# Optimization experiments

Measured on AMD Instinct MI355X. Metric: run time of the kernel, lower is better.

Reference implementation:

```python
import jax, jax.numpy as jnp
import numpy as np

M, K, N, R = 8192, 4096, 4096, 64  # tokens, in_features, out_features, pod_rank


def _unpack_int4(packed):
    """Unpack bytes (stored as int32 in [0,256)) into signed int4 values in [-8,7].
    Low nibble is element 2k, high nibble is element 2k+1."""
    b = packed.astype(jnp.int32)
    low = ((b & 0xF) ^ 8) - 8
    high = (((b >> 4) & 0xF) ^ 8) - 8
    out = jnp.stack([low, high], axis=-1)
    return out.reshape(packed.shape[:-1] + (packed.shape[-1] * 2,))


def setup_inputs() -> dict:
    key = jax.random.key(0)
    ks = jax.random.split(key, 7)
    x_quant = jax.random.randint(ks[0], (M, K // 2), 0, 256, dtype=jnp.int32)
    x_scale = jax.random.uniform(ks[1], (M,), dtype=jnp.float32) * 0.01 + 1e-4
    weight = jax.random.randint(ks[2], (N, K // 2), 0, 256, dtype=jnp.int32)
    weight_scales = jax.random.uniform(ks[3], (N, 1), dtype=jnp.float32) * 0.01 + 1e-4
    bias = jax.random.normal(ks[4], (N,), dtype=jnp.float32) * 0.02
    x_r = jax.random.normal(ks[5], (M, R), dtype=jnp.float32)
    w_outlier = jax.random.normal(ks[6], (N, R), dtype=jnp.float32) * 0.02
    return {"x_quant": x_quant, "x_scale": x_scale, "weight": weight,
            "weight_scales": weight_scales, "bias": bias, "x_r": x_r,
            "w_outlier": w_outlier}


def reference(x_quant, x_scale, weight, weight_scales, bias, x_r, w_outlier):
    xi = _unpack_int4(x_quant)          # [M, K] int32 in [-8,7]
    wi = _unpack_int4(weight)           # [N, K] int32 in [-8,7]
    y_int = jnp.matmul(xi, wi.T)        # [M, N] int32 accumulator
    # dequant: per-token activation scale * per-channel weight scale, plus bias
    y = (y_int.astype(jnp.float32) * x_scale[:, None] * weight_scales.reshape(1, -1)
         + bias[None, :])
    # fused low-rank outlier correction: addmm_(x_r, w_outlier.T)
    y = y + jnp.matmul(x_r, w_outlier.T)
    return y
```

## Files before the change

kernel.cpp:

```cpp
#include <hip/hip_runtime.h>
#include <hip/hip_fp16.h>

typedef int      v4i __attribute__((ext_vector_type(4)));
typedef int      v2i __attribute__((ext_vector_type(2)));
typedef float    v4f __attribute__((ext_vector_type(4)));
typedef _Float16 v8h __attribute__((ext_vector_type(8)));
typedef _Float16 v4h __attribute__((ext_vector_type(4)));

#define MDIM 8192
#define NDIM 4096
#define KDIM 4096
#define RDIM 64
#define KW   (KDIM / 2)
#define NT   (KDIM / 128)

typedef const __attribute__((address_space(1))) char* gas_ptr;
typedef __attribute__((address_space(3))) char*       las_ptr;

__device__ __forceinline__ void unpack_w(v4i w, int& lo8, int& hi8) {
    unsigned p01 = __builtin_amdgcn_perm((unsigned)w.y, (unsigned)w.x, 0x0C0C0400u);
    unsigned p23 = __builtin_amdgcn_perm((unsigned)w.w, (unsigned)w.z, 0x0C0C0400u);
    unsigned b4  = __builtin_amdgcn_perm(p23, p01, 0x05040100u);
    unsigned lo = b4 & 0x0F0F0F0Fu;
    unsigned hi = (b4 >> 4) & 0x0F0F0F0Fu;
    lo8 = (int)(((lo ^ 0x08080808u) + 0x78787878u) ^ 0x80808080u);
    hi8 = (int)(((hi ^ 0x08080808u) + 0x78787878u) ^ 0x80808080u);
}

__global__ __launch_bounds__(256)
void repack_int4(const int* __restrict__ xq, const int* __restrict__ wq,
                 char* __restrict__ x8, char* __restrict__ w8)
{
    const size_t XCH = (size_t)MDIM * KW / 4;
    const size_t TCH = XCH + (size_t)NDIM * KW / 4;
    size_t stride = (size_t)gridDim.x * blockDim.x;
    for (size_t i = (size_t)blockIdx.x * blockDim.x + threadIdx.x; i < TCH; i += stride) {
        const int* src;
        char* dst;
        if (i < XCH) { src = xq + i * 4; dst = x8 + i * 8; }
        else { size_t j = i - XCH; src = wq + j * 4; dst = w8 + j * 8; }
        v4i w = *(const v4i*)src;
        int lo8, hi8;
        unpack_w(w, lo8, hi8);
        *(v2i*)dst = (v2i){lo8, hi8};
    }
}

__device__ __forceinline__ void stage2(const char* g, char* l, int kt, int ks) {
    const char* s = g + kt * 128 + ks * 64;
    __builtin_amdgcn_global_load_lds((gas_ptr)(const void*)s,
                                     (las_ptr)(void*)l, 16, 0, 0);
    __builtin_amdgcn_global_load_lds((gas_ptr)(const void*)(s + (size_t)128 * KDIM),
                                     (las_ptr)(void*)(l + 8192), 16, 0, 0);
}

#define VM4 asm volatile("s_waitcnt vmcnt(4)" ::: "memory")
#define NOPW

#define PHASE(PAR, MH, KS, STAGE_STMT, WAIT_STMT) do {                          \
    const char* Ab = &Asub[PAR][KS][0];                                         \
    const char* Bb = &Bsub[PAR][KS][0];                                         \
    v4i a_[4], b_[4];                                                           \
    _Pragma("unroll")                                                           \
    for (int ii = 0; ii < 4; ++ii)                                              \
        a_[ii] = *(const v4i*)(Ab + aoff + ((MH) * 4 + ii) * 1024);             \
    _Pragma("unroll")                                                           \
    for (int jj = 0; jj < 4; ++jj)                                              \
        b_[jj] = *(const v4i*)(Bb + boff + jj * 1024);                          \
    STAGE_STMT;                                                                 \
    __builtin_amdgcn_s_barrier();                                               \
    __builtin_amdgcn_s_setprio(1);                                              \
    _Pragma("unroll")                                                           \
    for (int ii = 0; ii < 4; ++ii)                                              \
        _Pragma("unroll")                                                       \
        for (int jj = 0; jj < 4; ++jj)                                          \
            acc[(MH) * 4 + ii][jj] = __builtin_amdgcn_mfma_i32_16x16x64_i8(     \
                a_[ii], b_[jj], acc[(MH) * 4 + ii][jj], 0, 0, 0);               \
    __builtin_amdgcn_s_setprio(0);                                              \
    WAIT_STMT;                                                                  \
    asm volatile("s_barrier" ::: "memory");                                     \
} while (0)

__global__ __launch_bounds__(512, 2)
void w4a4_gemm8(const char* __restrict__ x8, const char* __restrict__ w8,
                const float* __restrict__ xsc, const float* __restrict__ wsc,
                const float* __restrict__ bias, const float* __restrict__ xr,
                const float* __restrict__ wo, float* __restrict__ out)
{
    __shared__ __align__(16) char Asub[2][2][16384];
    __shared__ __align__(16) char Bsub[2][2][16384];
    __shared__ float xs_s[256];
    __shared__ float ws_s[256];
    __shared__ float bs_s[256];

    const int tid  = threadIdx.x;
    const int lane = tid & 63;
    const int wid  = tid >> 6;
    const int wm   = wid >> 2;
    const int wn   = wid & 3;

    const int s  = (blockIdx.x & 7) * 64 + (blockIdx.x >> 3);
    const int by = s >> 4;
    const int bx = s & 15;

    if (tid < 256) {
        xs_s[tid] = xsc[by * 256 + tid];
    } else {
        int n = tid - 256;
        ws_s[n] = wsc[bx * 256 + n];
        bs_s[n] = bias[bx * 256 + n];
    }

    const int srow = wid * 16 + (lane >> 2);
    const int scol = ((lane & 3) * 16) ^ (((lane >> 3) & 3) << 4);
    const char* gA = x8 + (size_t)(by * 256 + srow) * KDIM + scol;
    const char* gB = w8 + (size_t)(bx * 256 + srow) * KDIM + scol;
    const int ldsW = wid * 1024;

    const int lr   = lane & 15;
    const int cef  = ((lane >> 4) << 4) ^ (((lr >> 1) & 3) << 4);
    const int aoff = (wm * 128 + lr) * 64 + cef;
    const int boff = (wn * 64  + lr) * 64 + cef;

    v4i acc[8][4];
#pragma unroll
    for (int i = 0; i < 8; ++i)
#pragma unroll
        for (int j = 0; j < 4; ++j) acc[i][j] = (v4i){0, 0, 0, 0};

    stage2(gA, &Asub[0][0][ldsW], 0, 0);
    stage2(gB, &Bsub[0][0][ldsW], 0, 0);
    stage2(gA, &Asub[0][1][ldsW], 0, 1);
    stage2(gB, &Bsub[0][1][ldsW], 0, 1);
    stage2(gA, &Asub[1][0][ldsW], 1, 0);
    stage2(gB, &Bsub[1][0][ldsW], 1, 0);
    asm volatile("s_waitcnt vmcnt(4)" ::: "memory");
    asm volatile("s_barrier" ::: "memory");

    for (int it = 0; it < NT / 2; ++it) {
        const int kt1 = 2 * it + 1;
        const int kt2 = (2 * it + 2 < NT) ? 2 * it + 2 : NT - 1;
        const int kt3 = (2 * it + 3 < NT) ? 2 * it + 3 : NT - 1;
        PHASE(0, 0, 0, stage2(gA, &Asub[1][1][ldsW], kt1, 1), NOPW);
        PHASE(0, 1, 0, stage2(gB, &Bsub[1][1][ldsW], kt1, 1), NOPW);
        PHASE(0, 0, 1, stage2(gA, &Asub[0][0][ldsW], kt2, 0), NOPW);
        PHASE(0, 1, 1, stage2(gB, &Bsub[0][0][ldsW], kt2, 0), VM4);
        PHASE(1, 0, 0, stage2(gA, &Asub[0][1][ldsW], kt2, 1), NOPW);
        PHASE(1, 1, 0, stage2(gB, &Bsub[0][1][ldsW], kt2, 1), NOPW);
        PHASE(1, 0, 1, stage2(gA, &Asub[1][0][ldsW], kt3, 0), NOPW);
        PHASE(1, 1, 1, stage2(gB, &Bsub[1][0][ldsW], kt3, 0), VM4);
    }

    asm volatile("s_waitcnt vmcnt(0)" ::: "memory");
    asm volatile("s_barrier" ::: "memory");

    _Float16* Xh = (_Float16*)&Asub[0][0][0];
    _Float16* Wh = (_Float16*)&Bsub[0][0][0];
    {
        const int rr = tid >> 3;
        const int c8 = (tid & 7) * 8;
#pragma unroll
        for (int p = 0; p < 4; ++p) {
            const int row = p * 64 + rr;
            v4f x0 = *(const v4f*)(xr + (size_t)(by * 256 + row) * RDIM + c8);
            v4f x1 = *(const v4f*)(xr + (size_t)(by * 256 + row) * RDIM + c8 + 4);
            v8h hx = {(_Float16)x0[0], (_Float16)x0[1], (_Float16)x0[2], (_Float16)x0[3],
                      (_Float16)x1[0], (_Float16)x1[1], (_Float16)x1[2], (_Float16)x1[3]};
            *(v8h*)((char*)Xh + (size_t)row * 144 + c8 * 2) = hx;
            v4f w0 = *(const v4f*)(wo + (size_t)(bx * 256 + row) * RDIM + c8);
            v4f w1 = *(const v4f*)(wo + (size_t)(bx * 256 + row) * RDIM + c8 + 4);
            v8h hw = {(_Float16)w0[0], (_Float16)w0[1], (_Float16)w0[2], (_Float16)w0[3],
                      (_Float16)w1[0], (_Float16)w1[1], (_Float16)w1[2], (_Float16)w1[3]};
            *(v8h*)((char*)Wh + (size_t)row * 144 + c8 * 2) = hw;
        }
    }

#pragma unroll
    for (int i = 0; i < 8; ++i) {
        const int r0 = wm * 128 + i * 16 + ((lane >> 4) << 2);
        const v4f xs4 = *(const v4f*)&xs_s[r0];
#pragma unroll
        for (int j = 0; j < 4; ++j) {
            const int col = wn * 64 + j * 16 + lr;
            const float sw = ws_s[col];
            const float bz = bs_s[col];
            v4f f;
#pragma unroll
            for (int r = 0; r < 4; ++r)
                f[r] = (float)acc[i][j][r] * xs4[r] * sw + bz;
            acc[i][j] = __builtin_bit_cast(v4i, f);
        }
    }
    __syncthreads();

#pragma unroll
    for (int ks = 0; ks < 2; ++ks) {
        v8h ah[8], bh[4];
#pragma unroll
        for (int i = 0; i < 8; ++i)
            ah[i] = *(const v8h*)((const char*)Xh +
                     (size_t)(wm * 128 + i * 16 + lr) * 144 + ks * 64 + ((lane >> 4) << 4));
#pragma unroll
        for (int j = 0; j < 4; ++j)
            bh[j] = *(const v8h*)((const char*)Wh +
                     (size_t)(wn * 64 + j * 16 + lr) * 144 + ks * 64 + ((lane >> 4) << 4));
#pragma unroll
        for (int i = 0; i < 8; ++i)
#pragma unroll
            for (int j = 0; j < 4; ++j) {
                v4f c = __builtin_bit_cast(v4f, acc[i][j]);
                c = __builtin_amdgcn_mfma_f32_16x16x32_f16(ah[i], bh[j], c, 0, 0, 0);
                acc[i][j] = __builtin_bit_cast(v4i, c);
            }
    }

    const size_t obase = (size_t)(by * 256 + wm * 128 + ((lane >> 4) << 2)) * NDIM
                       + bx * 256 + wn * 64 + lr;
#pragma unroll
    for (int i = 0; i < 8; ++i)
#pragma unroll
        for (int j = 0; j < 4; ++j) {
            v4f f = __builtin_bit_cast(v4f, acc[i][j]);
#pragma unroll
            for (int r = 0; r < 4; ++r)
                out[obase + (size_t)(i * 16 + r) * NDIM + j * 16] = f[r];
        }
}

__global__ __launch_bounds__(256, 2)
void w4a4_fused(const int* __restrict__ xq, const float* __restrict__ xsc,
                const int* __restrict__ wq, const float* __restrict__ wsc,
                const float* __restrict__ bias, const float* __restrict__ xr,
                const float* __restrict__ wo, float* __restrict__ out)
{
    __shared__ __align__(16) char As[128 * 144];
    __shared__ __align__(16) char Bs[128 * 144];
    __shared__ float xs_s[128];
    __shared__ float ws_s[128];
    __shared__ float bs_s[128];

    const int tid  = threadIdx.x;
    const int lane = tid & 63;
    const int wid  = tid >> 6;
    const int wm   = wid >> 1;
    const int wn   = wid & 1;
    const int bx   = blockIdx.x % (NDIM / 128);
    const int by   = blockIdx.x / (NDIM / 128);

    const int srow   = tid >> 4;
    const int schunk = tid & 15;

    if (tid < 128) {
        xs_s[tid] = xsc[by * 128 + tid];
    } else {
        int n = tid - 128;
        ws_s[n] = wsc[bx * 128 + n];
        bs_s[n] = bias[bx * 128 + n];
    }

    const int* gA = xq + (size_t)(by * 128 + srow) * KW + schunk * 4;
    const int* gB = wq + (size_t)(bx * 128 + srow) * KW + schunk * 4;
    char* lA = As + srow * 144 + schunk * 8;
    char* lB = Bs + srow * 144 + schunk * 8;

    v4i acc[4][4];
#pragma unroll
    for (int i = 0; i < 4; ++i)
#pragma unroll
        for (int j = 0; j < 4; ++j) acc[i][j] = (v4i){0, 0, 0, 0};

    const int lr = lane & 15;
    const int lkb = (lane >> 4) * 16;

    for (int kt = 0; kt < KDIM / 128; ++kt) {
#pragma unroll
        for (int p = 0; p < 8; ++p) {
            v4i w = *(const v4i*)(gA + (size_t)p * 16 * KW + kt * 64);
            int lo8, hi8;
            unpack_w(w, lo8, hi8);
            *(v2i*)(lA + p * 16 * 144) = (v2i){lo8, hi8};
        }
#pragma unroll
        for (int p = 0; p < 8; ++p) {
            v4i w = *(const v4i*)(gB + (size_t)p * 16 * KW + kt * 64);
            int lo8, hi8;
            unpack_w(w, lo8, hi8);
            *(v2i*)(lB + p * 16 * 144) = (v2i){lo8, hi8};
        }
        __syncthreads();
#pragma unroll
        for (int ks = 0; ks < 2; ++ks) {
            v4i av[4], bv[4];
#pragma unroll
            for (int i = 0; i < 4; ++i)
                av[i] = *(const v4i*)(As + (wm * 64 + i * 16 + lr) * 144 + ks * 64 + lkb);
#pragma unroll
            for (int j = 0; j < 4; ++j)
                bv[j] = *(const v4i*)(Bs + (wn * 64 + j * 16 + lr) * 144 + ks * 64 + lkb);
#pragma unroll
            for (int i = 0; i < 4; ++i)
#pragma unroll
                for (int j = 0; j < 4; ++j)
                    acc[i][j] = __builtin_amdgcn_mfma_i32_16x16x64_i8(av[i], bv[j], acc[i][j], 0, 0, 0);
        }
        __syncthreads();
    }

    _Float16* Xh = (_Float16*)As;
    _Float16* Wh = (_Float16*)Bs;
#pragma unroll
    for (int p = 0; p < 8; ++p) {
        int row = p * 16 + srow;
        float4 vx = *(const float4*)(xr + (size_t)(by * 128 + row) * RDIM + schunk * 4);
        *(v4h*)(Xh + row * 72 + schunk * 4) =
            (v4h){(_Float16)vx.x, (_Float16)vx.y, (_Float16)vx.z, (_Float16)vx.w};
        float4 vw = *(const float4*)(wo + (size_t)(bx * 128 + row) * RDIM + schunk * 4);
        *(v4h*)(Wh + row * 72 + schunk * 4) =
            (v4h){(_Float16)vw.x, (_Float16)vw.y, (_Float16)vw.z, (_Float16)vw.w};
    }
    __syncthreads();

    v4f facc[4][4];
#pragma unroll
    for (int i = 0; i < 4; ++i)
#pragma unroll
        for (int j = 0; j < 4; ++j) facc[i][j] = (v4f){0.f, 0.f, 0.f, 0.f};

    const int lkh = (lane >> 4) * 8;
#pragma unroll
    for (int ks = 0; ks < 2; ++ks) {
        v8h ah[4], bh[4];
#pragma unroll
        for (int i = 0; i < 4; ++i)
            ah[i] = *(const v8h*)(Xh + (wm * 64 + i * 16 + lr) * 72 + ks * 32 + lkh);
#pragma unroll
        for (int j = 0; j < 4; ++j)
            bh[j] = *(const v8h*)(Wh + (wn * 64 + j * 16 + lr) * 72 + ks * 32 + lkh);
#pragma unroll
        for (int i = 0; i < 4; ++i)
#pragma unroll
            for (int j = 0; j < 4; ++j)
                facc[i][j] = __builtin_amdgcn_mfma_f32_16x16x32_f16(ah[i], bh[j], facc[i][j], 0, 0, 0);
    }

#pragma unroll
    for (int i = 0; i < 4; ++i) {
        int row0 = wm * 64 + i * 16 + (lane >> 4) * 4;
#pragma unroll
        for (int j = 0; j < 4; ++j) {
            int col = wn * 64 + j * 16 + lr;
            float sw = ws_s[col];
            float bz = bs_s[col];
#pragma unroll
            for (int r = 0; r < 4; ++r) {
                int row = row0 + r;
                float v = (float)acc[i][j][r] * xs_s[row] * sw + bz + facc[i][j][r];
                out[(size_t)(by * 128 + row) * NDIM + (bx * 128 + col)] = v;
            }
        }
    }
}

extern "C" void kernel_launch(void* const* d_in, const int* in_sizes, int n_in,
                              void* d_out, int out_size, void* d_ws, size_t ws_size,
                              hipStream_t stream) {
    const int*   xq   = (const int*)d_in[0];
    const float* xsc  = (const float*)d_in[1];
    const int*   wq   = (const int*)d_in[2];
    const float* wsc  = (const float*)d_in[3];
    const float* bias = (const float*)d_in[4];
    const float* xr   = (const float*)d_in[5];
    const float* wo   = (const float*)d_in[6];
    float* out = (float*)d_out;

    const size_t X8 = (size_t)MDIM * KDIM;
    const size_t W8 = (size_t)NDIM * KDIM;

    if (ws_size >= X8 + W8) {
        char* x8 = (char*)d_ws;
        char* w8 = x8 + X8;
        repack_int4<<<2048, 256, 0, stream>>>(xq, wq, x8, w8);
        w4a4_gemm8<<<(MDIM / 256) * (NDIM / 256), 512, 0, stream>>>(
            x8, w8, xsc, wsc, bias, xr, wo, out);
    } else {
        w4a4_fused<<<(MDIM / 128) * (NDIM / 128), 256, 0, stream>>>(
            xq, xsc, wq, wsc, bias, xr, wo, out);
    }
}
```

Measured before the change: 172.6 us.

## Software-pipeline LDS fragment reads ahead of MFMA with register double-buffering

Restructures the main K loop so the LDS reads for the next phase are issued before the MFMAs of the current phase, using two register sets each for A and B. B fragments are reused across the two M halves instead of being reloaded every phase. The barrier count per phase drops from two to one, and the vmcnt waits are loosened to allow more global-to-LDS loads in flight. The cost is higher VGPR pressure under launch bounds (512,2), plus a risk of LDS hazards if the relaxed waits and single barriers do not fully order buffer reuse.

```diff
diff --git a/kernel.cpp b/kernel.cpp
--- a/kernel.cpp
+++ b/kernel.cpp
@@ -54,32 +54,30 @@
                                      (las_ptr)(void*)(l + 8192), 16, 0, 0);
 }
 
-#define VM4 asm volatile("s_waitcnt vmcnt(4)" ::: "memory")
-#define NOPW
-
-#define PHASE(PAR, MH, KS, STAGE_STMT, WAIT_STMT) do {                          \
-    const char* Ab = &Asub[PAR][KS][0];                                         \
-    const char* Bb = &Bsub[PAR][KS][0];                                         \
-    v4i a_[4], b_[4];                                                           \
-    _Pragma("unroll")                                                           \
-    for (int ii = 0; ii < 4; ++ii)                                              \
-        a_[ii] = *(const v4i*)(Ab + aoff + ((MH) * 4 + ii) * 1024);             \
-    _Pragma("unroll")                                                           \
-    for (int jj = 0; jj < 4; ++jj)                                              \
-        b_[jj] = *(const v4i*)(Bb + boff + jj * 1024);                          \
-    STAGE_STMT;                                                                 \
-    __builtin_amdgcn_s_barrier();                                               \
-    __builtin_amdgcn_s_setprio(1);                                              \
-    _Pragma("unroll")                                                           \
-    for (int ii = 0; ii < 4; ++ii)                                              \
-        _Pragma("unroll")                                                       \
-        for (int jj = 0; jj < 4; ++jj)                                          \
-            acc[(MH) * 4 + ii][jj] = __builtin_amdgcn_mfma_i32_16x16x64_i8(     \
-                a_[ii], b_[jj], acc[(MH) * 4 + ii][jj], 0, 0, 0);               \
-    __builtin_amdgcn_s_setprio(0);                                              \
-    WAIT_STMT;                                                                  \
-    asm volatile("s_barrier" ::: "memory");                                     \
-} while (0)
+#define BAR asm volatile("s_barrier" ::: "memory")
+#define VM6 asm volatile("s_waitcnt vmcnt(6)" ::: "memory")
+#define VM8 asm volatile("s_waitcnt vmcnt(8)" ::: "memory")
+
+#define READ_A(dst, PAR, KS, MH)                                               \
+    _Pragma("unroll")                                                          \
+    for (int ii = 0; ii < 4; ++ii)                                             \
+        dst[ii] = *(const v4i*)((const char*)Asub[PAR][KS] + aoff +            \
+                                ((MH) * 4 + ii) * 1024)
+
+#define READ_B(dst, PAR, KS)                                                   \
+    _Pragma("unroll")                                                          \
+    for (int jj = 0; jj < 4; ++jj)                                             \
+        dst[jj] = *(const v4i*)((const char*)Bsub[PAR][KS] + boff + jj * 1024)
+
+#define MMA(AS, BS, MH)                                                        \
+    __builtin_amdgcn_s_setprio(1);                                             \
+    _Pragma("unroll")                                                          \
+    for (int ii = 0; ii < 4; ++ii)                                             \
+        _Pragma("unroll")                                                      \
+        for (int jj = 0; jj < 4; ++jj)                                         \
+            acc[(MH) * 4 + ii][jj] = __builtin_amdgcn_mfma_i32_16x16x64_i8(    \
+                AS[ii], BS[jj], acc[(MH) * 4 + ii][jj], 0, 0, 0);              \
+    __builtin_amdgcn_s_setprio(0)
 
 __global__ __launch_bounds__(512, 2)
 void w4a4_gemm8(const char* __restrict__ x8, const char* __restrict__ w8,
@@ -134,25 +132,58 @@
     stage2(gB, &Bsub[0][1][ldsW], 0, 1);
     stage2(gA, &Asub[1][0][ldsW], 1, 0);
     stage2(gB, &Bsub[1][0][ldsW], 1, 0);
-    asm volatile("s_waitcnt vmcnt(4)" ::: "memory");
-    asm volatile("s_barrier" ::: "memory");
+    VM8;
+    BAR;
+
+    v4i a0[4], a1[4], b0[4], b1[4];
+    READ_A(a0, 0, 0, 0);
+    READ_B(b0, 0, 0);
 
     for (int it = 0; it < NT / 2; ++it) {
         const int kt1 = 2 * it + 1;
         const int kt2 = (2 * it + 2 < NT) ? 2 * it + 2 : NT - 1;
         const int kt3 = (2 * it + 3 < NT) ? 2 * it + 3 : NT - 1;
-        PHASE(0, 0, 0, stage2(gA, &Asub[1][1][ldsW], kt1, 1), NOPW);
-        PHASE(0, 1, 0, stage2(gB, &Bsub[1][1][ldsW], kt1, 1), NOPW);
-        PHASE(0, 0, 1, stage2(gA, &Asub[0][0][ldsW], kt2, 0), NOPW);
-        PHASE(0, 1, 1, stage2(gB, &Bsub[0][0][ldsW], kt2, 0), VM4);
-        PHASE(1, 0, 0, stage2(gA, &Asub[0][1][ldsW], kt2, 1), NOPW);
-        PHASE(1, 1, 0, stage2(gB, &Bsub[0][1][ldsW], kt2, 1), NOPW);
-        PHASE(1, 0, 1, stage2(gA, &Asub[1][0][ldsW], kt3, 0), NOPW);
-        PHASE(1, 1, 1, stage2(gB, &Bsub[1][0][ldsW], kt3, 0), VM4);
+
+        READ_A(a1, 0, 0, 1);
+        stage2(gA, &Asub[1][1][ldsW], kt1, 1);
+        MMA(a0, b0, 0);
+        VM6; BAR;
+        READ_A(a0, 0, 1, 0);
+        READ_B(b1, 0, 1);
+        stage2(gB, &Bsub[1][1][ldsW], kt1, 1);
+        MMA(a1, b0, 1);
+        BAR;
+        READ_A(a1, 0, 1, 1);
+        stage2(gA, &Asub[0][0][ldsW], kt2, 0);
+        MMA(a0, b1, 0);
+        VM6; BAR;
+        READ_A(a0, 1, 0, 0);
+        READ_B(b0, 1, 0);
+        stage2(gB, &Bsub[0][0][ldsW], kt2, 0);
+        MMA(a1, b1, 1);
+        BAR;
+        READ_A(a1, 1, 0, 1);
+        stage2(gA, &Asub[0][1][ldsW], kt2, 1);
+        MMA(a0, b0, 0);
+        VM6; BAR;
+        READ_A(a0, 1, 1, 0);
+        READ_B(b1, 1, 1);
+        stage2(gB, &Bsub[0][1][ldsW], kt2, 1);
+        MMA(a1, b0, 1);
+        BAR;
+        READ_A(a1, 1, 1, 1);
+        stage2(gA, &Asub[1][0][ldsW], kt3, 0);
+        MMA(a0, b1, 0);
+        VM6; BAR;
+        READ_A(a0, 0, 0, 0);
+        READ_B(b0, 0, 0);
+        stage2(gB, &Bsub[1][0][ldsW], kt3, 0);
+        MMA(a1, b1, 1);
+        BAR;
     }
 
     asm volatile("s_waitcnt vmcnt(0)" ::: "memory");
-    asm volatile("s_barrier" ::: "memory");
+    BAR;
 
     _Float16* Xh = (_Float16*)&Asub[0][0][0];
     _Float16* Wh = (_Float16*)&Bsub[0][0][0];
```

New measurement: 170.0 us. About the same (-1.5%).

## Double-buffer MFMA fragments in registers and interleave LDS reads via sched groups

Applied to the files above, without the earlier changes.

Replaces the eight half-tile phases per iteration, each with two barriers, with four quarter phases. Each phase prefetches the next K-slice's A and B fragments into a second register set while running 32 MFMAs on the current set, then waits once and hits a single barrier. sched_group_barrier hints interleave LDS reads and global-to-LDS loads between the MFMAs, and the s_setprio toggling is dropped. The goal is to hide LDS latency and halve barrier count, at the cost of many more live VGPRs, which risks spills under the 512-thread, 2-block launch bound.

```diff
diff --git a/kernel.cpp b/kernel.cpp
--- a/kernel.cpp
+++ b/kernel.cpp
@@ -54,31 +54,43 @@
                                      (las_ptr)(void*)(l + 8192), 16, 0, 0);
 }
 
+#define BAR asm volatile("s_barrier" ::: "memory")
 #define VM4 asm volatile("s_waitcnt vmcnt(4)" ::: "memory")
-#define NOPW
-
-#define PHASE(PAR, MH, KS, STAGE_STMT, WAIT_STMT) do {                          \
-    const char* Ab = &Asub[PAR][KS][0];                                         \
-    const char* Bb = &Bsub[PAR][KS][0];                                         \
-    v4i a_[4], b_[4];                                                           \
-    _Pragma("unroll")                                                           \
-    for (int ii = 0; ii < 4; ++ii)                                              \
-        a_[ii] = *(const v4i*)(Ab + aoff + ((MH) * 4 + ii) * 1024);             \
-    _Pragma("unroll")                                                           \
-    for (int jj = 0; jj < 4; ++jj)                                              \
-        b_[jj] = *(const v4i*)(Bb + boff + jj * 1024);                          \
-    STAGE_STMT;                                                                 \
-    __builtin_amdgcn_s_barrier();                                               \
-    __builtin_amdgcn_s_setprio(1);                                              \
-    _Pragma("unroll")                                                           \
-    for (int ii = 0; ii < 4; ++ii)                                              \
-        _Pragma("unroll")                                                       \
-        for (int jj = 0; jj < 4; ++jj)                                          \
-            acc[(MH) * 4 + ii][jj] = __builtin_amdgcn_mfma_i32_16x16x64_i8(     \
-                a_[ii], b_[jj], acc[(MH) * 4 + ii][jj], 0, 0, 0);               \
-    __builtin_amdgcn_s_setprio(0);                                              \
-    WAIT_STMT;                                                                  \
-    asm volatile("s_barrier" ::: "memory");                                     \
+#define SGB(m, n) __builtin_amdgcn_sched_group_barrier(m, n, 0)
+
+#define SGBSEQ do {                                                            \
+    SGB(0x100, 2); SGB(0x8, 4); SGB(0x100, 2); SGB(0x8, 4);                    \
+    SGB(0x100, 2); SGB(0x8, 4); SGB(0x100, 2); SGB(0x8, 4);                    \
+    SGB(0x100, 2); SGB(0x8, 4); SGB(0x100, 2); SGB(0x8, 4);                    \
+    SGB(0x30, 2);  SGB(0x8, 4); SGB(0x30, 2);  SGB(0x8, 4);                    \
+} while (0)
+
+#define READ_A8(dst, PAR, KS)                                                  \
+    _Pragma("unroll")                                                          \
+    for (int ii = 0; ii < 8; ++ii)                                             \
+        dst[ii] = *(const v4i*)((const char*)Asub[PAR][KS] + aoff + ii * 1024)
+
+#define READ_B4(dst, PAR, KS)                                                  \
+    _Pragma("unroll")                                                          \
+    for (int jj = 0; jj < 4; ++jj)                                             \
+        dst[jj] = *(const v4i*)((const char*)Bsub[PAR][KS] + boff + jj * 1024)
+
+#define MMA32(AS, BS)                                                          \
+    _Pragma("unroll")                                                          \
+    for (int ii = 0; ii < 8; ++ii)                                             \
+        _Pragma("unroll")                                                      \
+        for (int jj = 0; jj < 4; ++jj)                                         \
+            acc[ii][jj] = __builtin_amdgcn_mfma_i32_16x16x64_i8(               \
+                AS[ii], BS[jj], acc[ii][jj], 0, 0, 0)
+
+#define QPHASE(CA, CB, NA, NB, NPAR, NKS, SPAR, SKS, SKT) do {                 \
+    READ_A8(NA, NPAR, NKS);                                                    \
+    READ_B4(NB, NPAR, NKS);                                                    \
+    stage2(gA, &Asub[SPAR][SKS][ldsW], SKT, SKS);                              \
+    stage2(gB, &Bsub[SPAR][SKS][ldsW], SKT, SKS);                              \
+    MMA32(CA, CB);                                                             \
+    SGBSEQ;                                                                    \
+    VM4; BAR;                                                                  \
 } while (0)
 
 __global__ __launch_bounds__(512, 2)
@@ -101,20 +113,20 @@
 
     const int s  = (blockIdx.x & 7) * 64 + (blockIdx.x >> 3);
     const int by = s >> 4;
-    const int bx = s & 15;
+    const int bxn = s & 15;
 
     if (tid < 256) {
         xs_s[tid] = xsc[by * 256 + tid];
     } else {
         int n = tid - 256;
-        ws_s[n] = wsc[bx * 256 + n];
-        bs_s[n] = bias[bx * 256 + n];
+        ws_s[n] = wsc[bxn * 256 + n];
+        bs_s[n] = bias[bxn * 256 + n];
     }
 
     const int srow = wid * 16 + (lane >> 2);
     const int scol = ((lane & 3) * 16) ^ (((lane >> 3) & 3) << 4);
     const char* gA = x8 + (size_t)(by * 256 + srow) * KDIM + scol;
-    const char* gB = w8 + (size_t)(bx * 256 + srow) * KDIM + scol;
+    const char* gB = w8 + (size_t)(bxn * 256 + srow) * KDIM + scol;
     const int ldsW = wid * 1024;
 
     const int lr   = lane & 15;
@@ -134,25 +146,25 @@
     stage2(gB, &Bsub[0][1][ldsW], 0, 1);
     stage2(gA, &Asub[1][0][ldsW], 1, 0);
     stage2(gB, &Bsub[1][0][ldsW], 1, 0);
-    asm volatile("s_waitcnt vmcnt(4)" ::: "memory");
-    asm volatile("s_barrier" ::: "memory");
+    VM4;
+    BAR;
+
+    v4i fa0[8], fb0[4], fa1[8], fb1[4];
+    READ_A8(fa0, 0, 0);
+    READ_B4(fb0, 0, 0);
 
     for (int it = 0; it < NT / 2; ++it) {
         const int kt1 = 2 * it + 1;
         const int kt2 = (2 * it + 2 < NT) ? 2 * it + 2 : NT - 1;
         const int kt3 = (2 * it + 3 < NT) ? 2 * it + 3 : NT - 1;
-        PHASE(0, 0, 0, stage2(gA, &Asub[1][1][ldsW], kt1, 1), NOPW);
-        PHASE(0, 1, 0, stage2(gB, &Bsub[1][1][ldsW], kt1, 1), NOPW);
-        PHASE(0, 0, 1, stage2(gA, &Asub[0][0][ldsW], kt2, 0), NOPW);
-        PHASE(0, 1, 1, stage2(gB, &Bsub[0][0][ldsW], kt2, 0), VM4);
-        PHASE(1, 0, 0, stage2(gA, &Asub[0][1][ldsW], kt2, 1), NOPW);
-        PHASE(1, 1, 0, stage2(gB, &Bsub[0][1][ldsW], kt2, 1), NOPW);
-        PHASE(1, 0, 1, stage2(gA, &Asub[1][0][ldsW], kt3, 0), NOPW);
-        PHASE(1, 1, 1, stage2(gB, &Bsub[1][0][ldsW], kt3, 0), VM4);
+        QPHASE(fa0, fb0, fa1, fb1, 0, 1, 1, 1, kt1);
+        QPHASE(fa1, fb1, fa0, fb0, 1, 0, 0, 0, kt2);
+        QPHASE(fa0, fb0, fa1, fb1, 1, 1, 0, 1, kt2);
+        QPHASE(fa1, fb1, fa0, fb0, 0, 0, 1, 0, kt3);
     }
 
     asm volatile("s_waitcnt vmcnt(0)" ::: "memory");
-    asm volatile("s_barrier" ::: "memory");
+    BAR;
 
     _Float16* Xh = (_Float16*)&Asub[0][0][0];
     _Float16* Wh = (_Float16*)&Bsub[0][0][0];
@@ -167,8 +179,8 @@
             v8h hx = {(_Float16)x0[0], (_Float16)x0[1], (_Float16)x0[2], (_Float16)x0[3],
                       (_Float16)x1[0], (_Float16)x1[1], (_Float16)x1[2], (_Float16)x1[3]};
             *(v8h*)((char*)Xh + (size_t)row * 144 + c8 * 2) = hx;
-            v4f w0 = *(const v4f*)(wo + (size_t)(bx * 256 + row) * RDIM + c8);
-            v4f w1 = *(const v4f*)(wo + (size_t)(bx * 256 + row) * RDIM + c8 + 4);
+            v4f w0 = *(const v4f*)(wo + (size_t)(bxn * 256 + row) * RDIM + c8);
+            v4f w1 = *(const v4f*)(wo + (size_t)(bxn * 256 + row) * RDIM + c8 + 4);
             v8h hw = {(_Float16)w0[0], (_Float16)w0[1], (_Float16)w0[2], (_Float16)w0[3],
                       (_Float16)w1[0], (_Float16)w1[1], (_Float16)w1[2], (_Float16)w1[3]};
             *(v8h*)((char*)Wh + (size_t)row * 144 + c8 * 2) = hw;
@@ -215,7 +227,7 @@
     }
 
     const size_t obase = (size_t)(by * 256 + wm * 128 + ((lane >> 4) << 2)) * NDIM
-                       + bx * 256 + wn * 64 + lr;
+                       + bxn * 256 + wn * 64 + lr;
 #pragma unroll
     for (int i = 0; i < 8; ++i)
 #pragma unroll
```

After: 168.4 us. 1.02x faster.
